# Kernel optimization log

Measured on AMD Instinct MI355X. Metric: run time of the kernel, lower is better.

## Reference

```python
import jax, jax.numpy as jnp
import numpy as np

SEC = 20  # keypoints per section (hard-coded in original: i*20:(i+1)*20)


def smooth_l1(x):
    ax = jnp.abs(x)
    return jnp.where(ax < 1.0, 0.5 * x * x, ax - 0.5)


def setup_inputs() -> dict:
    key = jax.random.key(0)
    k1, k2, k3, k4 = jax.random.split(key, 4)
    B, K, NS = 8192, 400, 20
    return {
        "pred_keypoints": jax.random.normal(k1, (B, K, 3), dtype=jnp.float32),
        "gt_keypoints": jax.random.normal(k2, (B, K, 3), dtype=jnp.float32),
        "pred_section_logits": jax.random.normal(k3, (B, K, NS), dtype=jnp.float32),
        "gt_section_label": jax.random.randint(k4, (B, K), 0, NS, dtype=jnp.int64),
    }


def reference(pred_keypoints, gt_keypoints, pred_section_logits, gt_section_label):
    alpha, beta, delta, epsilon = 1.0, 4.0, 5.0, 6.0
    B, K, _ = pred_keypoints.shape
    S = K // SEC  # num sections

    keypoint_loss = jnp.mean(smooth_l1(pred_keypoints - gt_keypoints))

    # cross entropy over flattened [B*K, NS]
    logp = jax.nn.log_softmax(pred_section_logits, axis=-1)
    nll = -jnp.take_along_axis(logp, gt_section_label[..., None], axis=-1)[..., 0]
    section_loss = jnp.mean(nll)

    # per-section Procrustes alignment, batched over (B, S)
    P = pred_keypoints.reshape(B, S, SEC, 3)
    G = gt_keypoints.reshape(B, S, SEC, 3)
    Pc = P - P.mean(axis=2, keepdims=True)
    Gc = G - G.mean(axis=2, keepdims=True)
    # H = gt_centered^T @ pred_centered -> [B, S, 3, 3]
    H = jnp.einsum('bski,bskj->bsij', Gc, Pc)
    U, _, Vh = jnp.linalg.svd(H)  # torch.svd gives V with H = U diag(s) V^T; Vh = V^T
    R = jnp.einsum('bsik,bskj->bsij', U, Vh)  # U @ V^T
    P_aligned = jnp.einsum('bski,bsij->bskj', Pc, R)
    # sum of per-section means / S == overall mean (equal-size sections)
    rot_loss = jnp.mean(smooth_l1(P_aligned - Gc))

    # center alignment loss
    cent_loss = jnp.mean(smooth_l1(P.mean(axis=2) - G.mean(axis=2)))

    total = alpha * section_loss + beta * keypoint_loss + delta * rot_loss + epsilon * cent_loss
    return total
```

## Files before the change

### kernel.cpp

```cpp
#include <hip/hip_runtime.h>
#include <math.h>

static constexpr int Bn    = 8192;
static constexpr int Kn    = 400;
static constexpr int Sn    = 20;
static constexpr int NROWS = Bn * Kn;
static constexpr int NGRP  = Bn * Sn;

static constexpr int CE_BLOCKS = 2560;
static constexpr int CE_ROWS_PER_BLOCK = 1280;
static constexpr int PR_BLOCKS = 640,  PR_TPB = 256;
static constexpr int FUSED_BLOCKS = CE_BLOCKS + PR_BLOCKS;

static constexpr int WS_CE   = 0;
static constexpr int WS_KP   = 4096;
static constexpr int WS_ROT  = 8192;
static constexpr int WS_CENT = 12288;

__device__ __forceinline__ float smooth_l1f(float x) {
    float ax = fabsf(x);
    return ax < 1.0f ? 0.5f * x * x : ax - 0.5f;
}

__global__ __launch_bounds__(256) void fused_kernel(
    const float* __restrict__ logits,
    const int*   __restrict__ labels,
    const float* __restrict__ P,
    const float* __restrict__ G,
    float*       __restrict__ ws)
{
    const int t   = threadIdx.x;
    const int bid = blockIdx.x;
    const int lane = t & 63, wid = t >> 6;
    __shared__ float lbuf[2][5120];
    __shared__ float sm[3][4];

    if ((bid % 5) != 4) {
        const int cb = (bid / 5) * 4 + (bid % 5);
        const size_t blockRow0 = (size_t)cb * CE_ROWS_PER_BLOCK;
        const float* __restrict__ gsrc = logits + blockRow0 * 20;

        float4 pf[5];
        auto load_chunk = [&](int c) {
            const float* p = gsrc + (size_t)c * 5120 + wid * 1280 + lane * 4;
#pragma unroll
            for (int i = 0; i < 5; i++)
                pf[i] = *reinterpret_cast<const float4*>(p + i * 256);
        };
        auto store_chunk = [&](int buf) {
#pragma unroll
            for (int i = 0; i < 5; i++)
                *reinterpret_cast<float4*>(&lbuf[buf][wid * 1280 + i * 256 + lane * 4]) = pf[i];
        };

        load_chunk(0);
        store_chunk(0);

        float acc = 0.0f;
#pragma unroll
        for (int c = 0; c < 5; c++) {
            if (c + 1 < 5) load_chunk(c + 1);

            const float4* rowp = reinterpret_cast<const float4*>(&lbuf[c & 1][t * 20]);
            float x[20];
#pragma unroll
            for (int i = 0; i < 5; i++) {
                float4 v = rowp[i];
                x[4*i+0] = v.x; x[4*i+1] = v.y; x[4*i+2] = v.z; x[4*i+3] = v.w;
            }
            int lab = labels[blockRow0 + c * 256 + t];
            float m = x[0];
#pragma unroll
            for (int j = 1; j < 20; j++) m = fmaxf(m, x[j]);
            float se = 0.0f, xl = 0.0f;
#pragma unroll
            for (int j = 0; j < 20; j++) {
                se += __expf(x[j] - m);
                xl = (j == lab) ? x[j] : xl;
            }
            acc += __logf(se) + m - xl;

            if (c + 1 < 5) store_chunk((c + 1) & 1);
        }

#pragma unroll
        for (int o = 32; o > 0; o >>= 1) acc += __shfl_down(acc, o);
        if (lane == 0) sm[0][wid] = acc;
        __syncthreads();
        if (t == 0) ws[WS_CE + cb] = sm[0][0] + sm[0][1] + sm[0][2] + sm[0][3];
        return;
    }

    const int pb  = bid / 5;
    const int grp = pb * PR_TPB + t;
    const float4* __restrict__ pp = reinterpret_cast<const float4*>(P) + (size_t)grp * 15;
    const float4* __restrict__ gg = reinterpret_cast<const float4*>(G) + (size_t)grp * 15;

    float kp = 0.0f;
    float sp0=0,sp1=0,sp2=0, sg0=0,sg1=0,sg2=0;
    float S00=0,S01=0,S02=0, S10=0,S11=0,S12=0, S20=0,S21=0,S22=0;
#pragma unroll
    for (int ch = 0; ch < 5; ch++) {
        float4 a0 = pp[3*ch+0], a1 = pp[3*ch+1], a2 = pp[3*ch+2];
        float4 b0 = gg[3*ch+0], b1 = gg[3*ch+1], b2 = gg[3*ch+2];
        float pv[12] = {a0.x,a0.y,a0.z,a0.w, a1.x,a1.y,a1.z,a1.w, a2.x,a2.y,a2.z,a2.w};
        float gv[12] = {b0.x,b0.y,b0.z,b0.w, b1.x,b1.y,b1.z,b1.w, b2.x,b2.y,b2.z,b2.w};
#pragma unroll
        for (int q = 0; q < 4; q++) {
            float p0 = pv[3*q+0], p1 = pv[3*q+1], p2 = pv[3*q+2];
            float g0 = gv[3*q+0], g1 = gv[3*q+1], g2 = gv[3*q+2];
            kp += smooth_l1f(p0-g0) + smooth_l1f(p1-g1) + smooth_l1f(p2-g2);
            sp0 += p0; sp1 += p1; sp2 += p2;
            sg0 += g0; sg1 += g1; sg2 += g2;
            S00 += g0*p0; S01 += g0*p1; S02 += g0*p2;
            S10 += g1*p0; S11 += g1*p1; S12 += g1*p2;
            S20 += g2*p0; S21 += g2*p1; S22 += g2*p2;
        }
    }
    const float inv20 = 1.0f / 20.0f;
    float mp[3] = {sp0*inv20, sp1*inv20, sp2*inv20};
    float mg[3] = {sg0*inv20, sg1*inv20, sg2*inv20};
    float cent = smooth_l1f(mp[0]-mg[0]) + smooth_l1f(mp[1]-mg[1]) + smooth_l1f(mp[2]-mg[2]);

    float X[3][3];
    X[0][0] = S00 - 20.0f*mg[0]*mp[0];  X[0][1] = S01 - 20.0f*mg[0]*mp[1];  X[0][2] = S02 - 20.0f*mg[0]*mp[2];
    X[1][0] = S10 - 20.0f*mg[1]*mp[0];  X[1][1] = S11 - 20.0f*mg[1]*mp[1];  X[1][2] = S12 - 20.0f*mg[1]*mp[2];
    X[2][0] = S20 - 20.0f*mg[2]*mp[0];  X[2][1] = S21 - 20.0f*mg[2]*mp[1];  X[2][2] = S22 - 20.0f*mg[2]*mp[2];

#pragma unroll
    for (int it = 0; it < 8; it++) {
        float c00 =  X[1][1]*X[2][2] - X[1][2]*X[2][1];
        float c01 = -(X[1][0]*X[2][2] - X[1][2]*X[2][0]);
        float c02 =  X[1][0]*X[2][1] - X[1][1]*X[2][0];
        float c10 = -(X[0][1]*X[2][2] - X[0][2]*X[2][1]);
        float c11 =  X[0][0]*X[2][2] - X[0][2]*X[2][0];
        float c12 = -(X[0][0]*X[2][1] - X[0][1]*X[2][0]);
        float c20 =  X[0][1]*X[1][2] - X[0][2]*X[1][1];
        float c21 = -(X[0][0]*X[1][2] - X[0][2]*X[1][0]);
        float c22 =  X[0][0]*X[1][1] - X[0][1]*X[1][0];
        float d = X[0][0]*c00 + X[0][1]*c01 + X[0][2]*c02;
        float ad = fmaxf(fabsf(d), 1e-30f);
        float gam = __powf(ad, -(1.0f/3.0f));
        float dsn = (d < 0.0f) ? -ad : ad;
        float k1 = 0.5f * gam;
        float k2 = 0.5f / (gam * dsn);
        X[0][0] = k1*X[0][0] + k2*c00;  X[0][1] = k1*X[0][1] + k2*c01;  X[0][2] = k1*X[0][2] + k2*c02;
        X[1][0] = k1*X[1][0] + k2*c10;  X[1][1] = k1*X[1][1] + k2*c11;  X[1][2] = k1*X[1][2] + k2*c12;
        X[2][0] = k1*X[2][0] + k2*c20;  X[2][1] = k1*X[2][1] + k2*c21;  X[2][2] = k1*X[2][2] + k2*c22;
    }
    float s9 = X[0][0]+X[0][1]+X[0][2]+X[1][0]+X[1][1]+X[1][2]+X[2][0]+X[2][1]+X[2][2];
    if (!(s9 == s9) || fabsf(s9) > 1e10f) {
        X[0][0]=1; X[0][1]=0; X[0][2]=0;
        X[1][0]=0; X[1][1]=1; X[1][2]=0;
        X[2][0]=0; X[2][1]=0; X[2][2]=1;
    }

    float rot = 0.0f;
#pragma unroll
    for (int ch = 0; ch < 5; ch++) {
        float4 a0 = pp[3*ch+0], a1 = pp[3*ch+1], a2 = pp[3*ch+2];
        float4 b0 = gg[3*ch+0], b1 = gg[3*ch+1], b2 = gg[3*ch+2];
        float pv[12] = {a0.x,a0.y,a0.z,a0.w, a1.x,a1.y,a1.z,a1.w, a2.x,a2.y,a2.z,a2.w};
        float gv[12] = {b0.x,b0.y,b0.z,b0.w, b1.x,b1.y,b1.z,b1.w, b2.x,b2.y,b2.z,b2.w};
#pragma unroll
        for (int q = 0; q < 4; q++) {
            float pc0 = pv[3*q+0]-mp[0], pc1 = pv[3*q+1]-mp[1], pc2 = pv[3*q+2]-mp[2];
            float gc0 = gv[3*q+0]-mg[0], gc1 = gv[3*q+1]-mg[1], gc2 = gv[3*q+2]-mg[2];
            float a0r = pc0*X[0][0] + pc1*X[1][0] + pc2*X[2][0] - gc0;
            float a1r = pc0*X[0][1] + pc1*X[1][1] + pc2*X[2][1] - gc1;
            float a2r = pc0*X[0][2] + pc1*X[1][2] + pc2*X[2][2] - gc2;
            rot += smooth_l1f(a0r) + smooth_l1f(a1r) + smooth_l1f(a2r);
        }
    }

#pragma unroll
    for (int o = 32; o > 0; o >>= 1) {
        kp   += __shfl_down(kp, o);
        rot  += __shfl_down(rot, o);
        cent += __shfl_down(cent, o);
    }
    if (lane == 0) { sm[0][wid] = kp; sm[1][wid] = rot; sm[2][wid] = cent; }
    __syncthreads();
    if (t == 0) {
        ws[WS_KP   + pb] = sm[0][0] + sm[0][1] + sm[0][2] + sm[0][3];
        ws[WS_ROT  + pb] = sm[1][0] + sm[1][1] + sm[1][2] + sm[1][3];
        ws[WS_CENT + pb] = sm[2][0] + sm[2][1] + sm[2][2] + sm[2][3];
    }
}

__global__ __launch_bounds__(256) void reduce_kernel(
    const float* __restrict__ ws, float* __restrict__ out)
{
    const int t = threadIdx.x;
    float s_ce = 0, s_kp = 0, s_rot = 0, s_cent = 0;
    for (int i = t; i < CE_BLOCKS; i += 256) s_ce += ws[WS_CE + i];
    for (int i = t; i < PR_BLOCKS; i += 256) {
        s_kp   += ws[WS_KP + i];
        s_rot  += ws[WS_ROT + i];
        s_cent += ws[WS_CENT + i];
    }
#pragma unroll
    for (int o = 32; o > 0; o >>= 1) {
        s_ce   += __shfl_down(s_ce, o);
        s_kp   += __shfl_down(s_kp, o);
        s_rot  += __shfl_down(s_rot, o);
        s_cent += __shfl_down(s_cent, o);
    }
    __shared__ float sm[4][4];
    int lane = t & 63, wid = t >> 6;
    if (lane == 0) { sm[0][wid]=s_ce; sm[1][wid]=s_kp; sm[2][wid]=s_rot; sm[3][wid]=s_cent; }
    __syncthreads();
    if (t == 0) {
        float ce   = (sm[0][0]+sm[0][1]+sm[0][2]+sm[0][3]) * (1.0f / (float)NROWS);
        float kp   = (sm[1][0]+sm[1][1]+sm[1][2]+sm[1][3]) * (1.0f / (float)(NROWS * 3));
        float rot  = (sm[2][0]+sm[2][1]+sm[2][2]+sm[2][3]) * (1.0f / (float)(NROWS * 3));
        float cent = (sm[3][0]+sm[3][1]+sm[3][2]+sm[3][3]) * (1.0f / (float)(NGRP * 3));
        out[0] = ce + 4.0f * kp + 5.0f * rot + 6.0f * cent;
    }
}

extern "C" void kernel_launch(void* const* d_in, const int* in_sizes, int n_in,
                              void* d_out, int out_size, void* d_ws, size_t ws_size,
                              hipStream_t stream) {
    const float* pred_kp = (const float*)d_in[0];
    const float* gt_kp   = (const float*)d_in[1];
    const float* logits  = (const float*)d_in[2];
    const int*   labels  = (const int*)d_in[3];
    float* out = (float*)d_out;
    float* ws  = (float*)d_ws;

    fused_kernel<<<FUSED_BLOCKS, 256, 0, stream>>>(logits, labels, pred_kp, gt_kp, ws);
    reduce_kernel<<<1, 256, 0, stream>>>(ws, out);
}
```

Measured before the change: 440.3 us.

## Stage Procrustes keypoints through LDS with coalesced loads and rebalance block mix

Procrustes blocks now cover 64 groups each. All 256 threads do coalesced scalar loads of the P and G tiles into shared memory, then 64 threads run the per-group math reading float4 rows from LDS. Before, each thread read its own strided 240-byte rows straight from global memory. The CE path drops its double buffer for a single per-wave region, and blocks alternate 1:1 between CE and Procrustes instead of 4:1. The trade-off is that three of four waves sit idle during the Procrustes compute, and the final reduction drops its cross-wave shared-memory step.

```diff
diff --git a/kernel.cpp b/kernel.cpp
--- a/kernel.cpp
+++ b/kernel.cpp
@@ -9,7 +9,7 @@
 
 static constexpr int CE_BLOCKS = 2560;
 static constexpr int CE_ROWS_PER_BLOCK = 1280;
-static constexpr int PR_BLOCKS = 640,  PR_TPB = 256;
+static constexpr int PR_BLOCKS = 2560;
 static constexpr int FUSED_BLOCKS = CE_BLOCKS + PR_BLOCKS;
 
 static constexpr int WS_CE   = 0;
@@ -32,11 +32,11 @@
     const int t   = threadIdx.x;
     const int bid = blockIdx.x;
     const int lane = t & 63, wid = t >> 6;
-    __shared__ float lbuf[2][5120];
-    __shared__ float sm[3][4];
-
-    if ((bid % 5) != 4) {
-        const int cb = (bid / 5) * 4 + (bid % 5);
+    __shared__ __align__(16) float lds[7680];
+    __shared__ float sm[4];
+
+    if ((bid & 1) == 0) {
+        const int cb = bid >> 1;
         const size_t blockRow0 = (size_t)cb * CE_ROWS_PER_BLOCK;
         const float* __restrict__ gsrc = logits + blockRow0 * 20;
 
@@ -47,21 +47,21 @@
             for (int i = 0; i < 5; i++)
                 pf[i] = *reinterpret_cast<const float4*>(p + i * 256);
         };
-        auto store_chunk = [&](int buf) {
+        auto store_chunk = [&]() {
 #pragma unroll
             for (int i = 0; i < 5; i++)
-                *reinterpret_cast<float4*>(&lbuf[buf][wid * 1280 + i * 256 + lane * 4]) = pf[i];
+                *reinterpret_cast<float4*>(&lds[wid * 1280 + i * 256 + lane * 4]) = pf[i];
         };
 
         load_chunk(0);
-        store_chunk(0);
+        store_chunk();
 
         float acc = 0.0f;
 #pragma unroll
         for (int c = 0; c < 5; c++) {
             if (c + 1 < 5) load_chunk(c + 1);
 
-            const float4* rowp = reinterpret_cast<const float4*>(&lbuf[c & 1][t * 20]);
+            const float4* rowp = reinterpret_cast<const float4*>(&lds[t * 20]);
             float x[20];
 #pragma unroll
             for (int i = 0; i < 5; i++) {
@@ -80,41 +80,55 @@
             }
             acc += __logf(se) + m - xl;
 
-            if (c + 1 < 5) store_chunk((c + 1) & 1);
+            if (c + 1 < 5) store_chunk();
         }
 
 #pragma unroll
         for (int o = 32; o > 0; o >>= 1) acc += __shfl_down(acc, o);
-        if (lane == 0) sm[0][wid] = acc;
+        if (lane == 0) sm[wid] = acc;
         __syncthreads();
-        if (t == 0) ws[WS_CE + cb] = sm[0][0] + sm[0][1] + sm[0][2] + sm[0][3];
+        if (t == 0) ws[WS_CE + cb] = sm[0] + sm[1] + sm[2] + sm[3];
         return;
     }
 
-    const int pb  = bid / 5;
-    const int grp = pb * PR_TPB + t;
-    const float4* __restrict__ pp = reinterpret_cast<const float4*>(P) + (size_t)grp * 15;
-    const float4* __restrict__ gg = reinterpret_cast<const float4*>(G) + (size_t)grp * 15;
+    const int pb = bid >> 1;
+    const size_t g0 = (size_t)pb * 64;
+    const float* __restrict__ Pg = P + g0 * 60;
+    const float* __restrict__ Gg = G + g0 * 60;
+
+    float vP[15], vG[15];
+#pragma unroll
+    for (int i = 0; i < 15; i++) { vP[i] = Pg[t + 256*i]; vG[i] = Gg[t + 256*i]; }
+#pragma unroll
+    for (int i = 0; i < 15; i++) {
+        lds[       t + 256*i] = vP[i];
+        lds[3840 + t + 256*i] = vG[i];
+    }
+    __syncthreads();
+    if (t >= 64) return;
+
+    const float4* __restrict__ pr = reinterpret_cast<const float4*>(&lds[t * 60]);
+    const float4* __restrict__ gr = reinterpret_cast<const float4*>(&lds[3840 + t * 60]);
 
     float kp = 0.0f;
     float sp0=0,sp1=0,sp2=0, sg0=0,sg1=0,sg2=0;
     float S00=0,S01=0,S02=0, S10=0,S11=0,S12=0, S20=0,S21=0,S22=0;
 #pragma unroll
     for (int ch = 0; ch < 5; ch++) {
-        float4 a0 = pp[3*ch+0], a1 = pp[3*ch+1], a2 = pp[3*ch+2];
-        float4 b0 = gg[3*ch+0], b1 = gg[3*ch+1], b2 = gg[3*ch+2];
+        float4 a0 = pr[3*ch+0], a1 = pr[3*ch+1], a2 = pr[3*ch+2];
+        float4 b0 = gr[3*ch+0], b1 = gr[3*ch+1], b2 = gr[3*ch+2];
         float pv[12] = {a0.x,a0.y,a0.z,a0.w, a1.x,a1.y,a1.z,a1.w, a2.x,a2.y,a2.z,a2.w};
         float gv[12] = {b0.x,b0.y,b0.z,b0.w, b1.x,b1.y,b1.z,b1.w, b2.x,b2.y,b2.z,b2.w};
 #pragma unroll
         for (int q = 0; q < 4; q++) {
             float p0 = pv[3*q+0], p1 = pv[3*q+1], p2 = pv[3*q+2];
-            float g0 = gv[3*q+0], g1 = gv[3*q+1], g2 = gv[3*q+2];
-            kp += smooth_l1f(p0-g0) + smooth_l1f(p1-g1) + smooth_l1f(p2-g2);
+            float g0v = gv[3*q+0], g1v = gv[3*q+1], g2v = gv[3*q+2];
+            kp += smooth_l1f(p0-g0v) + smooth_l1f(p1-g1v) + smooth_l1f(p2-g2v);
             sp0 += p0; sp1 += p1; sp2 += p2;
-            sg0 += g0; sg1 += g1; sg2 += g2;
-            S00 += g0*p0; S01 += g0*p1; S02 += g0*p2;
-            S10 += g1*p0; S11 += g1*p1; S12 += g1*p2;
-            S20 += g2*p0; S21 += g2*p1; S22 += g2*p2;
+            sg0 += g0v; sg1 += g1v; sg2 += g2v;
+            S00 += g0v*p0; S01 += g0v*p1; S02 += g0v*p2;
+            S10 += g1v*p0; S11 += g1v*p1; S12 += g1v*p2;
+            S20 += g2v*p0; S21 += g2v*p1; S22 += g2v*p2;
         }
     }
     const float inv20 = 1.0f / 20.0f;
@@ -158,8 +172,8 @@
     float rot = 0.0f;
 #pragma unroll
     for (int ch = 0; ch < 5; ch++) {
-        float4 a0 = pp[3*ch+0], a1 = pp[3*ch+1], a2 = pp[3*ch+2];
-        float4 b0 = gg[3*ch+0], b1 = gg[3*ch+1], b2 = gg[3*ch+2];
+        float4 a0 = pr[3*ch+0], a1 = pr[3*ch+1], a2 = pr[3*ch+2];
+        float4 b0 = gr[3*ch+0], b1 = gr[3*ch+1], b2 = gr[3*ch+2];
         float pv[12] = {a0.x,a0.y,a0.z,a0.w, a1.x,a1.y,a1.z,a1.w, a2.x,a2.y,a2.z,a2.w};
         float gv[12] = {b0.x,b0.y,b0.z,b0.w, b1.x,b1.y,b1.z,b1.w, b2.x,b2.y,b2.z,b2.w};
 #pragma unroll
@@ -179,12 +193,10 @@
         rot  += __shfl_down(rot, o);
         cent += __shfl_down(cent, o);
     }
-    if (lane == 0) { sm[0][wid] = kp; sm[1][wid] = rot; sm[2][wid] = cent; }
-    __syncthreads();
     if (t == 0) {
-        ws[WS_KP   + pb] = sm[0][0] + sm[0][1] + sm[0][2] + sm[0][3];
-        ws[WS_ROT  + pb] = sm[1][0] + sm[1][1] + sm[1][2] + sm[1][3];
-        ws[WS_CENT + pb] = sm[2][0] + sm[2][1] + sm[2][2] + sm[2][3];
+        ws[WS_KP   + pb] = kp;
+        ws[WS_ROT  + pb] = rot;
+        ws[WS_CENT + pb] = cent;
     }
 }
 
```

After: 459.1 us. +4.3%, slower.
